# Kernel optimization log

Hardware: AMD Instinct MI355X
Metric: run time of the kernel (lower is better)

Reference implementation:

```python
import jax, jax.numpy as jnp
import numpy as np

N_HEAD = 16
TOPK = 2


def _forward(x, noise, Wk, Wv, Wq, Wo, Wg, Wn):
    B, T, C = x.shape
    E = Wg.shape[1]
    H = N_HEAD
    D = C // H
    x2 = x.reshape(-1, C)  # [N, C], N = B*T
    # noisy gating: logits + randn * softplus(noise_proj)
    gate_logits = x2 @ Wg + noise * jax.nn.softplus(x2 @ Wn)  # [N, E]
    w, sel = jax.lax.top_k(gate_logits, TOPK)                 # [N, K]
    w = jax.nn.softmax(w.astype(jnp.float32), axis=1).astype(x.dtype)
    # shared keys/values across experts
    k = (x @ Wk).reshape(B, T, H, D)
    v = (x @ Wv).reshape(B, T, H, D)
    # per-expert queries for all tokens, gathered per selected expert below
    q_all = jnp.einsum('btc,eco->bteo', x, Wq)  # [B, T, E, C]
    causal = jnp.tril(jnp.ones((T, T), dtype=bool))  # key j visible to query t iff j <= t
    scale = 1.0 / np.sqrt(D).astype(np.float32)
    sel_bt = sel.reshape(B, T, TOPK)
    w_bt = w.reshape(B, T, TOPK)
    out = jnp.zeros_like(x)
    for s in range(TOPK):  # small fixed loop over top-k slots
        e = sel_bt[:, :, s]  # [B, T] expert id per token
        q = jnp.take_along_axis(q_all, e[:, :, None, None], axis=2)[:, :, 0, :]  # [B, T, C]
        qh = q.reshape(B, T, H, D)
        scores = jnp.einsum('bthd,bjhd->bhtj', qh, k) * scale  # [B, H, T, T]
        scores = jnp.where(causal[None, None], scores, -jnp.inf)
        p = jax.nn.softmax(scores, axis=-1)
        attn = jnp.einsum('bhtj,bjhd->bthd', p, v).reshape(B, T, C)
        o_all = jnp.einsum('btc,eco->bteo', attn, Wo)  # [B, T, E, C]
        o = jnp.take_along_axis(o_all, e[:, :, None, None], axis=2)[:, :, 0, :]
        out = out + w_bt[:, :, s:s + 1] * o
    return out


def setup_inputs() -> dict:
    key = jax.random.key(0)
    ks = jax.random.split(key, 8)
    B, T, C, E = 4, 1024, 1024, 8
    s = 0.02
    x = jax.random.normal(ks[0], (B, T, C), jnp.float32)
    noise = jax.random.normal(ks[1], (B * T, E), jnp.float32)
    Wk = jax.random.normal(ks[2], (C, C), jnp.float32) * s
    Wv = jax.random.normal(ks[3], (C, C), jnp.float32) * s
    Wq = jax.random.normal(ks[4], (E, C, C), jnp.float32) * s
    Wo = jax.random.normal(ks[5], (E, C, C), jnp.float32) * s
    Wg = jax.random.normal(ks[6], (C, E), jnp.float32) * s
    Wn = jax.random.normal(ks[7], (C, E), jnp.float32) * s
    return {'x': x, 'noise': noise, 'Wk': Wk, 'Wv': Wv, 'Wq': Wq, 'Wo': Wo, 'Wg': Wg, 'Wn': Wn}


def reference(x, noise, Wk, Wv, Wq, Wo, Wg, Wn):
    return _forward(x, noise, Wk, Wv, Wq, Wo, Wg, Wn)
```

## Files before the change

kernel.cpp:

```cpp
#include <hip/hip_runtime.h>
#include <hip/hip_bf16.h>

#define TSEQ   1024
#define NC     1024
#define MBT    4096
#define NEXP   8
#define NHEAD  16
#define DHEAD  64
#define PERM_CAP 10240
#define MAXTILES 96

typedef __attribute__((ext_vector_type(8))) short bf16x8;
typedef __attribute__((ext_vector_type(4))) float f32x4;

typedef __attribute__((address_space(3))) unsigned char* lds_ptr_t;
typedef const __attribute__((address_space(1))) unsigned char* glb_ptr_t;

static __device__ __forceinline__ void gload16(const void* g, void* l){
    __builtin_amdgcn_global_load_lds((glb_ptr_t)g, (lds_ptr_t)l, 16, 0, 0);
}

static __device__ __forceinline__ unsigned short f2bf(float x){
    unsigned int u = __float_as_uint(x);
    u += 0x7fff + ((u >> 16) & 1);
    return (unsigned short)(u >> 16);
}
static __device__ __forceinline__ unsigned int pk2bf(float a, float b){
    unsigned int ua = __float_as_uint(a), ub = __float_as_uint(b);
    ua += 0x7fff + ((ua >> 16) & 1);
    ub += 0x7fff + ((ub >> 16) & 1);
    return (ua >> 16) | (ub & 0xffff0000u);
}
static __device__ __forceinline__ float bf2f(unsigned short u){
    return __uint_as_float(((unsigned int)u) << 16);
}

__global__ __launch_bounds__(256)
void gate_kernel(const float* __restrict__ x, const float* __restrict__ noise,
                 const float* __restrict__ Wg, const float* __restrict__ Wn,
                 int* __restrict__ epair, float* __restrict__ wpair,
                 unsigned short* __restrict__ xb){
    int t = blockIdx.x*4 + (threadIdx.x >> 6);
    int lane = threadIdx.x & 63;
    float ag[8] = {0,0,0,0,0,0,0,0};
    float an[8] = {0,0,0,0,0,0,0,0};
    const float* xr = x + (size_t)t * NC;
    unsigned short* xbr = xb + (size_t)t * NC;
    for (int c = lane; c < NC; c += 64){
        float xv = xr[c];
        xbr[c] = f2bf(xv);
        #pragma unroll
        for (int j = 0; j < 8; j++){
            ag[j] = fmaf(xv, Wg[c*8 + j], ag[j]);
            an[j] = fmaf(xv, Wn[c*8 + j], an[j]);
        }
    }
    #pragma unroll
    for (int j = 0; j < 8; j++){
        #pragma unroll
        for (int o = 32; o >= 1; o >>= 1){
            ag[j] += __shfl_xor(ag[j], o, 64);
            an[j] += __shfl_xor(an[j], o, 64);
        }
    }
    if (lane == 0){
        float lg[8];
        #pragma unroll
        for (int j = 0; j < 8; j++){
            float z = an[j];
            float sp = (z > 20.f) ? z : log1pf(expf(z));
            lg[j] = ag[j] + noise[(size_t)t*8 + j] * sp;
        }
        int i0 = 0; float v0 = lg[0];
        #pragma unroll
        for (int j = 1; j < 8; j++) if (lg[j] > v0){ v0 = lg[j]; i0 = j; }
        int i1 = -1; float v1 = -3.4e38f;
        #pragma unroll
        for (int j = 0; j < 8; j++) if (j != i0 && lg[j] > v1){ v1 = lg[j]; i1 = j; }
        float e1 = expf(v1 - v0);
        float w0 = 1.f / (1.f + e1);
        epair[2*t]   = i0;
        epair[2*t+1] = i1;
        wpair[2*t]   = w0;
        wpair[2*t+1] = e1 * w0;
    }
}

__global__ void prep_w(const float* __restrict__ Wk, const float* __restrict__ Wv,
                       const float* __restrict__ Wq, const float* __restrict__ Wo,
                       unsigned short* __restrict__ Wkvt, unsigned short* __restrict__ Wqt,
                       unsigned short* __restrict__ Wot){
    __shared__ float t[32][33];
    int z = blockIdx.z;
    const float* src; unsigned short* dst;
    if (z == 0){ src = Wk; dst = Wkvt; }
    else if (z == 1){ src = Wv; dst = Wkvt + (size_t)NC*NC; }
    else if (z < 10){ src = Wq + (size_t)(z-2)*NC*NC; dst = Wqt + (size_t)(z-2)*NC*NC; }
    else { src = Wo + (size_t)(z-10)*NC*NC; dst = Wot + (size_t)(z-10)*NC*NC; }
    int k0 = blockIdx.x * 32, n0 = blockIdx.y * 32;
    int tx = threadIdx.x, ty = threadIdx.y;
    #pragma unroll
    for (int i = 0; i < 4; i++)
        t[ty + i*8][tx] = src[(size_t)(k0 + ty + i*8)*NC + n0 + tx];
    __syncthreads();
    #pragma unroll
    for (int i = 0; i < 4; i++)
        dst[(size_t)(n0 + ty + i*8)*NC + k0 + tx] = f2bf(t[tx][ty + i*8]);
}

__global__ void group_build(const int* __restrict__ epair, int* __restrict__ cursor,
                            int* __restrict__ tile_g, int* __restrict__ tile_pos,
                            int* __restrict__ ntiles, int* __restrict__ perm){
    __shared__ int cnt[16];
    int tid = threadIdx.x;
    if (tid < 16) cnt[tid] = 0;
    __syncthreads();
    for (int p = tid; p < 2*MBT; p += 256){
        int g = ((p & 1) << 3) | epair[p];
        atomicAdd(&cnt[g], 1);
    }
    for (int i = tid; i < PERM_CAP; i += 256) perm[i] = -1;
    __syncthreads();
    if (tid == 0){
        int off = 0, tt = 0;
        for (int g = 0; g < 16; g++){
            int c = cnt[g];
            cursor[g] = off;
            int nt = (c + 127) >> 7;
            for (int i = 0; i < nt; i++){ tile_g[tt] = g; tile_pos[tt] = off + i*128; tt++; }
            off += nt << 7;
        }
        ntiles[0] = tt;
    }
}

__global__ __launch_bounds__(256)
void fill_perm(const int* __restrict__ epair, int* __restrict__ cursor,
               int* __restrict__ perm){
    int p = blockIdx.x * 256 + threadIdx.x;
    int lane = threadIdx.x & 63;
    int g = ((p & 1) << 3) | epair[p];
    unsigned long long ltmask = (lane == 63) ? 0x7fffffffffffffffull
                                             : (((unsigned long long)1 << lane) - 1);
    #pragma unroll 1
    for (int grp = 0; grp < 16; grp++){
        unsigned long long m = __ballot(g == grp);
        if (m == 0ull) continue;
        if (g == grp){
            int leader = __ffsll(m) - 1;
            int base = 0;
            if (lane == leader) base = atomicAdd(&cursor[grp], __popcll(m));
            base = __shfl(base, leader, 64);
            perm[base + __popcll(m & ltmask)] = p;
        }
    }
}

__global__ __launch_bounds__(256)
void gemm_fused(const unsigned short* __restrict__ xb,
                const unsigned short* __restrict__ Wkvt,
                const unsigned short* __restrict__ Wqt,
                unsigned short* __restrict__ kbuf,
                unsigned short* __restrict__ vbT,
                unsigned short* __restrict__ qselb,
                const int* __restrict__ perm,
                const int* __restrict__ tile_g,
                const int* __restrict__ tile_pos,
                const int* __restrict__ ntiles){
    int flat = blockIdx.x;
    bool isQ = (flat >= 512);
    int ntile, slot, tpos = 0;
    const unsigned short* bt;
    if (!isQ){
        ntile = flat & 15; slot = flat >> 4;
        bt = Wkvt;
    } else {
        int f2 = flat - 512;
        ntile = f2 & 7; slot = f2 >> 3;
        if (slot >= ntiles[0]) return;
        int g = tile_g[slot];
        bt = Wqt + (size_t)(g & 7) * NC * NC;
        tpos = tile_pos[slot];
    }

    __shared__ __align__(16) unsigned short smem[16896];
    unsigned short* As = smem;
    unsigned short* Bs = smem + 8192;

    int tid = threadIdx.x;
    int lane = tid & 63, wv = tid >> 6;
    int wr = wv >> 1, wc = wv & 1;
    int quad = lane >> 4, l15 = lane & 15;

    int laneR = lane >> 3;
    int swz = ((lane & 7) ^ (laneR & 7)) * 8;

    const unsigned short* ag[4];
    const unsigned short* bg[4];
    #pragma unroll
    for (int it = 0; it < 4; it++){
        int row = wv*32 + it*8 + laneR;
        if (!isQ){
            ag[it] = xb + (size_t)(slot*128 + row) * NC + swz;
        } else {
            int p = perm[tpos + row];
            if (p < 0) p = 0;
            ag[it] = xb + (size_t)(p >> 1) * NC + swz;
        }
        bg[it] = bt + (size_t)(ntile*128 + row) * NC + swz;
    }

    f32x4 acc[4][4];
    #pragma unroll
    for (int i = 0; i < 4; i++)
        #pragma unroll
        for (int j = 0; j < 4; j++) acc[i][j] = (f32x4){0.f,0.f,0.f,0.f};

    for (int kk = 0; kk < NC; kk += 64){
        #pragma unroll
        for (int it = 0; it < 4; it++){
            gload16(ag[it] + kk, &As[(wv*32 + it*8)*64]);
            gload16(bg[it] + kk, &Bs[(wv*32 + it*8)*64]);
        }
        __syncthreads();
        #pragma unroll
        for (int kh = 0; kh < 2; kh++){
            bf16x8 af[4], bfr[4];
            #pragma unroll
            for (int mi = 0; mi < 4; mi++)
                af[mi]  = *(const bf16x8*)&As[(wr*64 + mi*16 + l15)*64 + (((kh*4 + quad) ^ (l15 & 7))*8)];
            #pragma unroll
            for (int ni = 0; ni < 4; ni++)
                bfr[ni] = *(const bf16x8*)&Bs[(wc*64 + ni*16 + l15)*64 + (((kh*4 + quad) ^ (l15 & 7))*8)];
            #pragma unroll
            for (int mi = 0; mi < 4; mi++)
                #pragma unroll
                for (int ni = 0; ni < 4; ni++)
                    acc[mi][ni] = __builtin_amdgcn_mfma_f32_16x16x32_bf16(af[mi], bfr[ni], acc[mi][ni], 0, 0, 0);
        }
        __syncthreads();
    }

    bool isV = (!isQ) && (ntile >= 8);
    float scale = isQ ? 0.125f : 1.0f;
    if (!isV){
        #pragma unroll
        for (int mi = 0; mi < 4; mi++)
            #pragma unroll
            for (int ni = 0; ni < 4; ni++)
                #pragma unroll
                for (int r = 0; r < 4; r++)
                    smem[(wr*64 + mi*16 + quad*4 + r)*132 + wc*64 + ni*16 + l15] =
                        f2bf(scale * acc[mi][ni][r]);
        __syncthreads();
        #pragma unroll
        for (int cc = 0; cc < 8; cc++){
            int chunk = tid + cc*256;
            int row = chunk >> 4, c8 = (chunk & 15) * 8;
            uint4 v = *(const uint4*)&smem[row*132 + c8];
            if (!isQ){
                *(uint4*)(kbuf + (size_t)(slot*128 + row)*NC + ntile*128 + c8) = v;
            } else {
                int p = perm[tpos + row];
                if (p >= 0)
                    *(uint4*)(qselb + (size_t)p*NC + ntile*128 + c8) = v;
            }
        }
    } else {
        #pragma unroll
        for (int mi = 0; mi < 4; mi++)
            #pragma unroll
            for (int ni = 0; ni < 4; ni++){
                ushort4 pk;
                pk.x = f2bf(acc[mi][ni][0]);
                pk.y = f2bf(acc[mi][ni][1]);
                pk.z = f2bf(acc[mi][ni][2]);
                pk.w = f2bf(acc[mi][ni][3]);
                *(ushort4*)&smem[(wc*64 + ni*16 + l15)*132 + wr*64 + mi*16 + quad*4] = pk;
            }
        __syncthreads();
        int b = slot >> 3, t0 = (slot & 7)*128;
        int cvBase = (ntile - 8)*128;
        #pragma unroll
        for (int cc = 0; cc < 8; cc++){
            int chunk = tid + cc*256;
            int row = chunk >> 4, c8 = (chunk & 15) * 8;
            uint4 v = *(const uint4*)&smem[row*132 + c8];
            *(uint4*)(vbT + ((size_t)(b*NC + cvBase + row))*TSEQ + t0 + c8) = v;
        }
    }
}

__global__ __launch_bounds__(256)
void gemm_o(const unsigned short* __restrict__ A,
            const unsigned short* __restrict__ Bt,
            unsigned short* __restrict__ osb,
            const int* __restrict__ perm,
            const int* __restrict__ tile_g,
            const int* __restrict__ tile_pos,
            const int* __restrict__ ntiles){
    int ntile = blockIdx.x;
    int slot  = blockIdx.y;
    if (slot >= ntiles[0]) return;
    int g = tile_g[slot];
    const unsigned short* bt = Bt + (size_t)(g & 7) * NC * NC;
    int tpos = tile_pos[slot];

    __shared__ __align__(16) unsigned short smem[16896];
    unsigned short* As = smem;
    unsigned short* Bs = smem + 8192;

    int tid = threadIdx.x;
    int lane = tid & 63, wv = tid >> 6;
    int wr = wv >> 1, wc = wv & 1;
    int quad = lane >> 4, l15 = lane & 15;

    int laneR = lane >> 3;
    int swz = ((lane & 7) ^ (laneR & 7)) * 8;

    const unsigned short* ag[4];
    const unsigned short* bg[4];
    #pragma unroll
    for (int it = 0; it < 4; it++){
        int row = wv*32 + it*8 + laneR;
        int p = perm[tpos + row];
        if (p < 0) p = 0;
        ag[it] = A + (size_t)(p & 1) * MBT * NC + (size_t)(p >> 1) * NC + swz;
        bg[it] = bt + (size_t)(ntile*128 + row) * NC + swz;
    }

    f32x4 acc[4][4];
    #pragma unroll
    for (int i = 0; i < 4; i++)
        #pragma unroll
        for (int j = 0; j < 4; j++) acc[i][j] = (f32x4){0.f,0.f,0.f,0.f};

    for (int kk = 0; kk < NC; kk += 64){
        #pragma unroll
        for (int it = 0; it < 4; it++){
            gload16(ag[it] + kk, &As[(wv*32 + it*8)*64]);
            gload16(bg[it] + kk, &Bs[(wv*32 + it*8)*64]);
        }
        __syncthreads();
        #pragma unroll
        for (int kh = 0; kh < 2; kh++){
            bf16x8 af[4], bfr[4];
            #pragma unroll
            for (int mi = 0; mi < 4; mi++)
                af[mi]  = *(const bf16x8*)&As[(wr*64 + mi*16 + l15)*64 + (((kh*4 + quad) ^ (l15 & 7))*8)];
            #pragma unroll
            for (int ni = 0; ni < 4; ni++)
                bfr[ni] = *(const bf16x8*)&Bs[(wc*64 + ni*16 + l15)*64 + (((kh*4 + quad) ^ (l15 & 7))*8)];
            #pragma unroll
            for (int mi = 0; mi < 4; mi++)
                #pragma unroll
                for (int ni = 0; ni < 4; ni++)
                    acc[mi][ni] = __builtin_amdgcn_mfma_f32_16x16x32_bf16(af[mi], bfr[ni], acc[mi][ni], 0, 0, 0);
        }
        __syncthreads();
    }

    #pragma unroll
    for (int mi = 0; mi < 4; mi++)
        #pragma unroll
        for (int ni = 0; ni < 4; ni++)
            #pragma unroll
            for (int r = 0; r < 4; r++)
                smem[(wr*64 + mi*16 + quad*4 + r)*132 + wc*64 + ni*16 + l15] =
                    f2bf(acc[mi][ni][r]);
    __syncthreads();
    #pragma unroll
    for (int cc = 0; cc < 8; cc++){
        int chunk = tid + cc*256;
        int row = chunk >> 4, c8 = (chunk & 15) * 8;
        int p = perm[tpos + row];
        if (p >= 0){
            uint4 v = *(const uint4*)&smem[row*132 + c8];
            *(uint4*)(osb + ((size_t)(p & 1)*MBT + (p >> 1))*NC + ntile*128 + c8) = v;
        }
    }
}

__global__ __launch_bounds__(256)
void combine(const unsigned short* __restrict__ os, const float* __restrict__ wpair,
             float* __restrict__ out){
    size_t flat = ((size_t)blockIdx.x * 256 + threadIdx.x) * 8;
    int t = (int)(flat >> 10);
    float w0 = wpair[2*t], w1 = wpair[2*t+1];
    bf16x8 a = *(const bf16x8*)(os + flat);
    bf16x8 b = *(const bf16x8*)(os + (size_t)MBT*NC + flat);
    float4 r0, r1;
    r0.x = w0*bf2f((unsigned short)a[0]) + w1*bf2f((unsigned short)b[0]);
    r0.y = w0*bf2f((unsigned short)a[1]) + w1*bf2f((unsigned short)b[1]);
    r0.z = w0*bf2f((unsigned short)a[2]) + w1*bf2f((unsigned short)b[2]);
    r0.w = w0*bf2f((unsigned short)a[3]) + w1*bf2f((unsigned short)b[3]);
    r1.x = w0*bf2f((unsigned short)a[4]) + w1*bf2f((unsigned short)b[4]);
    r1.y = w0*bf2f((unsigned short)a[5]) + w1*bf2f((unsigned short)b[5]);
    r1.z = w0*bf2f((unsigned short)a[6]) + w1*bf2f((unsigned short)b[6]);
    r1.w = w0*bf2f((unsigned short)a[7]) + w1*bf2f((unsigned short)b[7]);
    *(float4*)(out + flat)     = r0;
    *(float4*)(out + flat + 4) = r1;
}

__global__ __launch_bounds__(256)
void attn_k(const unsigned short* __restrict__ qsel, const unsigned short* __restrict__ kb,
            const unsigned short* __restrict__ vbT, unsigned short* __restrict__ attnb){
    int b = blockIdx.y >> 4, h = blockIdx.y & 15;
    int s = blockIdx.z;
    int tid = threadIdx.x, lane = tid & 63, wv = tid >> 6;
    int quad = lane >> 4, l15 = lane & 15;
    int laneR = lane >> 3;
    int swz = ((lane & 7) ^ (laneR & 7)) * 8;

    __shared__ __align__(16) unsigned short ksh[64*64];
    __shared__ __align__(16) unsigned short vsh[64*64];
    __shared__ __align__(16) unsigned short pwork[4][32][72];

    #pragma unroll
    for (int half = 0; half < 2; half++){
        int qb = half ? (7 - blockIdx.x) : blockIdx.x;
        int qbase = qb*128 + wv*32;
        int ig[2] = { qbase + l15, qbase + 16 + l15 };

        bf16x8 qf[2][2];
        #pragma unroll
        for (int isub = 0; isub < 2; isub++){
            const unsigned short* qrow = qsel + (((size_t)(b*TSEQ + qbase + isub*16 + l15))*2 + s)*NC + h*DHEAD;
            qf[isub][0] = *(const bf16x8*)(qrow + quad*8);
            qf[isub][1] = *(const bf16x8*)(qrow + 32 + quad*8);
        }

        float lrun[2] = {0.f, 0.f};
        f32x4 oacc[4][2];
        #pragma unroll
        for (int d = 0; d < 4; d++)
            #pragma unroll
            for (int i = 0; i < 2; i++) oacc[d][i] = (f32x4){0.f,0.f,0.f,0.f};

        int njt = qb*2 + 2;
        for (int jt = 0; jt < njt; jt++){
            #pragma unroll
            for (int it = 0; it < 2; it++){
                int r = wv*16 + it*8 + laneR;
                gload16(kb  + ((size_t)(b*TSEQ + jt*64 + r))*NC + h*DHEAD + swz,
                        &ksh[(wv*16 + it*8)*64]);
                gload16(vbT + ((size_t)(b*NC + h*DHEAD + r))*TSEQ + jt*64 + swz,
                        &vsh[(wv*16 + it*8)*64]);
            }
            __syncthreads();

            if (jt*64 <= qbase + 31){
                f32x4 sac[4][2];
                #pragma unroll
                for (int jsub = 0; jsub < 4; jsub++){
                    bf16x8 kf0 = *(const bf16x8*)&ksh[(jsub*16 + l15)*64 + ((quad     ^ (l15 & 7))*8)];
                    bf16x8 kf1 = *(const bf16x8*)&ksh[(jsub*16 + l15)*64 + (((4+quad) ^ (l15 & 7))*8)];
                    #pragma unroll
                    for (int isub = 0; isub < 2; isub++){
                        f32x4 z = (f32x4){0.f,0.f,0.f,0.f};
                        z = __builtin_amdgcn_mfma_f32_16x16x32_bf16(kf0, qf[isub][0], z, 0, 0, 0);
                        z = __builtin_amdgcn_mfma_f32_16x16x32_bf16(kf1, qf[isub][1], z, 0, 0, 0);
                        sac[jsub][isub] = z;
                    }
                }
                if (jt*64 + 63 > qbase){
                    #pragma unroll
                    for (int jsub = 0; jsub < 4; jsub++)
                        #pragma unroll
                        for (int r = 0; r < 4; r++){
                            int j = jt*64 + jsub*16 + quad*4 + r;
                            #pragma unroll
                            for (int isub = 0; isub < 2; isub++)
                                if (j > ig[isub]) sac[jsub][isub][r] = -1e30f;
                        }
                }
                #pragma unroll
                for (int isub = 0; isub < 2; isub++){
                    float rs = 0.f;
                    #pragma unroll
                    for (int jsub = 0; jsub < 4; jsub++){
                        float p0 = __expf(sac[jsub][isub][0]);
                        float p1 = __expf(sac[jsub][isub][1]);
                        float p2 = __expf(sac[jsub][isub][2]);
                        float p3 = __expf(sac[jsub][isub][3]);
                        rs += (p0 + p1) + (p2 + p3);
                        uint2 pk;
                        pk.x = pk2bf(p0, p1);
                        pk.y = pk2bf(p2, p3);
                        *(uint2*)&pwork[wv][isub*16 + l15][jsub*16 + quad*4] = pk;
                    }
                    rs += __shfl_xor(rs, 16, 64);
                    rs += __shfl_xor(rs, 32, 64);
                    lrun[isub] += rs;
                }
                bf16x8 pf[2][2];
                #pragma unroll
                for (int kh = 0; kh < 2; kh++)
                    #pragma unroll
                    for (int isub = 0; isub < 2; isub++)
                        pf[kh][isub] = *(const bf16x8*)&pwork[wv][isub*16 + l15][kh*32 + quad*8];
                #pragma unroll
                for (int dsub = 0; dsub < 4; dsub++){
                    bf16x8 vf0 = *(const bf16x8*)&vsh[(dsub*16 + l15)*64 + ((quad     ^ (l15 & 7))*8)];
                    bf16x8 vf1 = *(const bf16x8*)&vsh[(dsub*16 + l15)*64 + (((4+quad) ^ (l15 & 7))*8)];
                    #pragma unroll
                    for (int isub = 0; isub < 2; isub++){
                        oacc[dsub][isub] = __builtin_amdgcn_mfma_f32_16x16x32_bf16(vf0, pf[0][isub], oacc[dsub][isub], 0, 0, 0);
                        oacc[dsub][isub] = __builtin_amdgcn_mfma_f32_16x16x32_bf16(vf1, pf[1][isub], oacc[dsub][isub], 0, 0, 0);
                    }
                }
            }
            __syncthreads();
        }

        float inv[2] = { 1.f / lrun[0], 1.f / lrun[1] };
        #pragma unroll
        for (int dsub = 0; dsub < 4; dsub++)
            #pragma unroll
            for (int isub = 0; isub < 2; isub++){
                uint2 ov;
                ov.x = pk2bf(oacc[dsub][isub][0] * inv[isub], oacc[dsub][isub][1] * inv[isub]);
                ov.y = pk2bf(oacc[dsub][isub][2] * inv[isub], oacc[dsub][isub][3] * inv[isub]);
                *(uint2*)&pwork[wv][isub*16 + l15][dsub*16 + quad*4] = ov;
            }
        #pragma unroll
        for (int rr = 0; rr < 4; rr++){
            int idx = rr*64 + lane;
            int il = idx >> 3, cc = (idx & 7) * 8;
            int t = qb*128 + wv*32 + il;
            *(uint4*)(attnb + (size_t)s*MBT*NC + ((size_t)(b*TSEQ + t))*NC + h*DHEAD + cc) =
                *(const uint4*)&pwork[wv][il][cc];
        }
    }
}

extern "C" void kernel_launch(void* const* d_in, const int* in_sizes, int n_in,
                              void* d_out, int out_size, void* d_ws, size_t ws_size,
                              hipStream_t stream){
    (void)in_sizes; (void)n_in; (void)out_size; (void)ws_size;
    const float* x     = (const float*)d_in[0];
    const float* noise = (const float*)d_in[1];
    const float* Wk    = (const float*)d_in[2];
    const float* Wv    = (const float*)d_in[3];
    const float* Wq    = (const float*)d_in[4];
    const float* Wo    = (const float*)d_in[5];
    const float* Wg    = (const float*)d_in[6];
    const float* Wn    = (const float*)d_in[7];
    float* out = (float*)d_out;

    char* ws = (char*)d_ws;
    size_t off = 0;
    auto alloc = [&](size_t bytes) -> void* {
        void* p = ws + off;
        off += (bytes + 255) & ~(size_t)255;
        return p;
    };
    unsigned short* xb    = (unsigned short*)alloc((size_t)MBT*NC*2);
    unsigned short* vbufT = (unsigned short*)alloc((size_t)MBT*NC*2);
    unsigned short* kbuf  = (unsigned short*)alloc((size_t)MBT*NC*2);
    unsigned short* qselb = (unsigned short*)alloc((size_t)MBT*2*NC*2);
    unsigned short* attnb = (unsigned short*)alloc((size_t)2*MBT*NC*2);
    unsigned short* Wkvt  = (unsigned short*)alloc((size_t)2*NC*NC*2);
    unsigned short* Wqt   = (unsigned short*)alloc((size_t)NEXP*NC*NC*2);
    unsigned short* Wot   = (unsigned short*)alloc((size_t)NEXP*NC*NC*2);
    int*   epair   = (int*)alloc(2*MBT*4);
    float* wpair   = (float*)alloc(2*MBT*4);
    int*   perm    = (int*)alloc(PERM_CAP*4);
    int*   cursor  = (int*)alloc(16*4);
    int*   tile_g  = (int*)alloc(MAXTILES*4);
    int*   tile_pos= (int*)alloc(MAXTILES*4);
    int*   ntiles  = (int*)alloc(4);

    unsigned short* osb = qselb;

    prep_w<<<dim3(32,32,18), dim3(32,8), 0, stream>>>(Wk, Wv, Wq, Wo, Wkvt, Wqt, Wot);
    gate_kernel<<<1024, 256, 0, stream>>>(x, noise, Wg, Wn, epair, wpair, xb);
    group_build<<<1, 256, 0, stream>>>(epair, cursor, tile_g, tile_pos, ntiles, perm);
    fill_perm<<<32, 256, 0, stream>>>(epair, cursor, perm);

    gemm_fused<<<1280, 256, 0, stream>>>(xb, Wkvt, Wqt, kbuf, vbufT, qselb,
                                         perm, tile_g, tile_pos, ntiles);

    attn_k<<<dim3(4,64,2), 256, 0, stream>>>(qselb, kbuf, vbufT, attnb);

    gemm_o<<<dim3(8,MAXTILES), 256, 0, stream>>>(attnb, Wot, osb, perm, tile_g, tile_pos, ntiles);
    combine<<<2048, 256, 0, stream>>>(osb, wpair, out);
}
```

Before: 347.0 us.

## Double-buffer LDS tiles in GEMM and attention kernels; merge weight prep with gating

```diff
diff --git a/kernel.cpp b/kernel.cpp
--- a/kernel.cpp
+++ b/kernel.cpp
@@ -36,12 +36,37 @@
 }
 
 __global__ __launch_bounds__(256)
-void gate_kernel(const float* __restrict__ x, const float* __restrict__ noise,
-                 const float* __restrict__ Wg, const float* __restrict__ Wn,
-                 int* __restrict__ epair, float* __restrict__ wpair,
-                 unsigned short* __restrict__ xb){
-    int t = blockIdx.x*4 + (threadIdx.x >> 6);
-    int lane = threadIdx.x & 63;
+void prep_gate(const float* __restrict__ Wk, const float* __restrict__ Wv,
+               const float* __restrict__ Wq, const float* __restrict__ Wo,
+               unsigned short* __restrict__ Wkvt, unsigned short* __restrict__ Wqt,
+               unsigned short* __restrict__ Wot,
+               const float* __restrict__ x, const float* __restrict__ noise,
+               const float* __restrict__ Wg, const float* __restrict__ Wn,
+               int* __restrict__ epair, float* __restrict__ wpair,
+               unsigned short* __restrict__ xb){
+    int z = blockIdx.z;
+    int tx = threadIdx.x, ty = threadIdx.y;
+    if (z < 18){
+        __shared__ float t[32][33];
+        const float* src; unsigned short* dst;
+        if (z == 0){ src = Wk; dst = Wkvt; }
+        else if (z == 1){ src = Wv; dst = Wkvt + (size_t)NC*NC; }
+        else if (z < 10){ src = Wq + (size_t)(z-2)*NC*NC; dst = Wqt + (size_t)(z-2)*NC*NC; }
+        else { src = Wo + (size_t)(z-10)*NC*NC; dst = Wot + (size_t)(z-10)*NC*NC; }
+        int k0 = blockIdx.x * 32, n0 = blockIdx.y * 32;
+        #pragma unroll
+        for (int i = 0; i < 4; i++)
+            t[ty + i*8][tx] = src[(size_t)(k0 + ty + i*8)*NC + n0 + tx];
+        __syncthreads();
+        #pragma unroll
+        for (int i = 0; i < 4; i++)
+            dst[(size_t)(n0 + ty + i*8)*NC + k0 + tx] = f2bf(t[tx][ty + i*8]);
+        return;
+    }
+    int flat = ty*32 + tx;
+    int blk = blockIdx.y*32 + blockIdx.x;
+    int t = blk*4 + (flat >> 6);
+    int lane = flat & 63;
     float ag[8] = {0,0,0,0,0,0,0,0};
     float an[8] = {0,0,0,0,0,0,0,0};
     const float* xr = x + (size_t)t * NC;
@@ -67,8 +92,8 @@
         float lg[8];
         #pragma unroll
         for (int j = 0; j < 8; j++){
-            float z = an[j];
-            float sp = (z > 20.f) ? z : log1pf(expf(z));
+            float z2 = an[j];
+            float sp = (z2 > 20.f) ? z2 : log1pf(expf(z2));
             lg[j] = ag[j] + noise[(size_t)t*8 + j] * sp;
         }
         int i0 = 0; float v0 = lg[0];
@@ -84,28 +109,6 @@
         wpair[2*t]   = w0;
         wpair[2*t+1] = e1 * w0;
     }
-}
-
-__global__ void prep_w(const float* __restrict__ Wk, const float* __restrict__ Wv,
-                       const float* __restrict__ Wq, const float* __restrict__ Wo,
-                       unsigned short* __restrict__ Wkvt, unsigned short* __restrict__ Wqt,
-                       unsigned short* __restrict__ Wot){
-    __shared__ float t[32][33];
-    int z = blockIdx.z;
-    const float* src; unsigned short* dst;
-    if (z == 0){ src = Wk; dst = Wkvt; }
-    else if (z == 1){ src = Wv; dst = Wkvt + (size_t)NC*NC; }
-    else if (z < 10){ src = Wq + (size_t)(z-2)*NC*NC; dst = Wqt + (size_t)(z-2)*NC*NC; }
-    else { src = Wo + (size_t)(z-10)*NC*NC; dst = Wot + (size_t)(z-10)*NC*NC; }
-    int k0 = blockIdx.x * 32, n0 = blockIdx.y * 32;
-    int tx = threadIdx.x, ty = threadIdx.y;
-    #pragma unroll
-    for (int i = 0; i < 4; i++)
-        t[ty + i*8][tx] = src[(size_t)(k0 + ty + i*8)*NC + n0 + tx];
-    __syncthreads();
-    #pragma unroll
-    for (int i = 0; i < 4; i++)
-        dst[(size_t)(n0 + ty + i*8)*NC + k0 + tx] = f2bf(t[tx][ty + i*8]);
 }
 
 __global__ void group_build(const int* __restrict__ epair, int* __restrict__ cursor,
@@ -155,6 +158,8 @@
         }
     }
 }
+
+#define AB 8192
 
 __global__ __launch_bounds__(256)
 void gemm_fused(const unsigned short* __restrict__ xb,
@@ -183,10 +188,7 @@
         tpos = tile_pos[slot];
     }
 
-    __shared__ __align__(16) unsigned short smem[16896];
-    unsigned short* As = smem;
-    unsigned short* Bs = smem + 8192;
-
+    __shared__ __align__(16) unsigned short smem[4*AB];
     int tid = threadIdx.x;
     int lane = tid & 63, wv = tid >> 6;
     int wr = wv >> 1, wc = wv & 1;
@@ -216,13 +218,24 @@
         #pragma unroll
         for (int j = 0; j < 4; j++) acc[i][j] = (f32x4){0.f,0.f,0.f,0.f};
 
+    #pragma unroll
+    for (int it = 0; it < 4; it++){
+        gload16(ag[it], &smem[(wv*32 + it*8)*64]);
+        gload16(bg[it], &smem[AB + (wv*32 + it*8)*64]);
+    }
+    int cur = 0;
     for (int kk = 0; kk < NC; kk += 64){
-        #pragma unroll
-        for (int it = 0; it < 4; it++){
-            gload16(ag[it] + kk, &As[(wv*32 + it*8)*64]);
-            gload16(bg[it] + kk, &Bs[(wv*32 + it*8)*64]);
-        }
         __syncthreads();
+        if (kk + 64 < NC){
+            int nb = (cur ^ 1) * 2 * AB;
+            #pragma unroll
+            for (int it = 0; it < 4; it++){
+                gload16(ag[it] + kk + 64, &smem[nb + (wv*32 + it*8)*64]);
+                gload16(bg[it] + kk + 64, &smem[nb + AB + (wv*32 + it*8)*64]);
+            }
+        }
+        const unsigned short* As = &smem[cur*2*AB];
+        const unsigned short* Bs = &smem[cur*2*AB + AB];
         #pragma unroll
         for (int kh = 0; kh < 2; kh++){
             bf16x8 af[4], bfr[4];
@@ -238,8 +251,9 @@
                 for (int ni = 0; ni < 4; ni++)
                     acc[mi][ni] = __builtin_amdgcn_mfma_f32_16x16x32_bf16(af[mi], bfr[ni], acc[mi][ni], 0, 0, 0);
         }
-        __syncthreads();
-    }
+        cur ^= 1;
+    }
+    __syncthreads();
 
     bool isV = (!isQ) && (ntile >= 8);
     float scale = isQ ? 0.125f : 1.0f;
@@ -306,10 +320,7 @@
     const unsigned short* bt = Bt + (size_t)(g & 7) * NC * NC;
     int tpos = tile_pos[slot];
 
-    __shared__ __align__(16) unsigned short smem[16896];
-    unsigned short* As = smem;
-    unsigned short* Bs = smem + 8192;
-
+    __shared__ __align__(16) unsigned short smem[4*AB];
     int tid = threadIdx.x;
     int lane = tid & 63, wv = tid >> 6;
     int wr = wv >> 1, wc = wv & 1;
@@ -335,13 +346,24 @@
         #pragma unroll
         for (int j = 0; j < 4; j++) acc[i][j] = (f32x4){0.f,0.f,0.f,0.f};
 
+    #pragma unroll
+    for (int it = 0; it < 4; it++){
+        gload16(ag[it], &smem[(wv*32 + it*8)*64]);
+        gload16(bg[it], &smem[AB + (wv*32 + it*8)*64]);
+    }
+    int cur = 0;
     for (int kk = 0; kk < NC; kk += 64){
-        #pragma unroll
-        for (int it = 0; it < 4; it++){
-            gload16(ag[it] + kk, &As[(wv*32 + it*8)*64]);
-            gload16(bg[it] + kk, &Bs[(wv*32 + it*8)*64]);
-        }
         __syncthreads();
+        if (kk + 64 < NC){
+            int nb = (cur ^ 1) * 2 * AB;
+            #pragma unroll
+            for (int it = 0; it < 4; it++){
+                gload16(ag[it] + kk + 64, &smem[nb + (wv*32 + it*8)*64]);
+                gload16(bg[it] + kk + 64, &smem[nb + AB + (wv*32 + it*8)*64]);
+            }
+        }
+        const unsigned short* As = &smem[cur*2*AB];
+        const unsigned short* Bs = &smem[cur*2*AB + AB];
         #pragma unroll
         for (int kh = 0; kh < 2; kh++){
             bf16x8 af[4], bfr[4];
@@ -357,8 +379,9 @@
                 for (int ni = 0; ni < 4; ni++)
                     acc[mi][ni] = __builtin_amdgcn_mfma_f32_16x16x32_bf16(af[mi], bfr[ni], acc[mi][ni], 0, 0, 0);
         }
-        __syncthreads();
-    }
+        cur ^= 1;
+    }
+    __syncthreads();
 
     #pragma unroll
     for (int mi = 0; mi < 4; mi++)
@@ -402,6 +425,8 @@
     *(float4*)(out + flat + 4) = r1;
 }
 
+#define KVB 4096
+
 __global__ __launch_bounds__(256)
 void attn_k(const unsigned short* __restrict__ qsel, const unsigned short* __restrict__ kb,
             const unsigned short* __restrict__ vbT, unsigned short* __restrict__ attnb){
@@ -412,8 +437,7 @@
     int laneR = lane >> 3;
     int swz = ((lane & 7) ^ (laneR & 7)) * 8;
 
-    __shared__ __align__(16) unsigned short ksh[64*64];
-    __shared__ __align__(16) unsigned short vsh[64*64];
+    __shared__ __align__(16) unsigned short kv[4*KVB];
     __shared__ __align__(16) unsigned short pwork[4][32][72];
 
     #pragma unroll
@@ -438,79 +462,93 @@
             for (int i = 0; i < 2; i++) oacc[d][i] = (f32x4){0.f,0.f,0.f,0.f};
 
         int njt = qb*2 + 2;
+        __syncthreads();
+        #pragma unroll
+        for (int it = 0; it < 2; it++){
+            int r = wv*16 + it*8 + laneR;
+            gload16(kb  + ((size_t)(b*TSEQ + r))*NC + h*DHEAD + swz,
+                    &kv[(wv*16 + it*8)*64]);
+            gload16(vbT + ((size_t)(b*NC + h*DHEAD + r))*TSEQ + swz,
+                    &kv[2*KVB + (wv*16 + it*8)*64]);
+        }
+        int cur = 0;
         for (int jt = 0; jt < njt; jt++){
-            #pragma unroll
-            for (int it = 0; it < 2; it++){
-                int r = wv*16 + it*8 + laneR;
-                gload16(kb  + ((size_t)(b*TSEQ + jt*64 + r))*NC + h*DHEAD + swz,
-                        &ksh[(wv*16 + it*8)*64]);
-                gload16(vbT + ((size_t)(b*NC + h*DHEAD + r))*TSEQ + jt*64 + swz,
-                        &vsh[(wv*16 + it*8)*64]);
-            }
             __syncthreads();
-
-            if (jt*64 <= qbase + 31){
-                f32x4 sac[4][2];
+            if (jt + 1 < njt){
+                int nb = (cur ^ 1) * KVB;
+                #pragma unroll
+                for (int it = 0; it < 2; it++){
+                    int r = wv*16 + it*8 + laneR;
+                    gload16(kb  + ((size_t)(b*TSEQ + (jt+1)*64 + r))*NC + h*DHEAD + swz,
+                            &kv[nb + (wv*16 + it*8)*64]);
+                    gload16(vbT + ((size_t)(b*NC + h*DHEAD + r))*TSEQ + (jt+1)*64 + swz,
+                            &kv[nb + 2*KVB + (wv*16 + it*8)*64]);
+                }
+            }
+            const unsigned short* ksh = &kv[cur*KVB];
+            const unsigned short* vsh = &kv[cur*KVB + 2*KVB];
+            cur ^= 1;
+
+            if (jt*64 > qbase + 31) continue;
+            f32x4 sac[4][2];
+            #pragma unroll
+            for (int jsub = 0; jsub < 4; jsub++){
+                bf16x8 kf0 = *(const bf16x8*)&ksh[(jsub*16 + l15)*64 + ((quad     ^ (l15 & 7))*8)];
+                bf16x8 kf1 = *(const bf16x8*)&ksh[(jsub*16 + l15)*64 + (((4+quad) ^ (l15 & 7))*8)];
+                #pragma unroll
+                for (int isub = 0; isub < 2; isub++){
+                    f32x4 z = (f32x4){0.f,0.f,0.f,0.f};
+                    z = __builtin_amdgcn_mfma_f32_16x16x32_bf16(kf0, qf[isub][0], z, 0, 0, 0);
+                    z = __builtin_amdgcn_mfma_f32_16x16x32_bf16(kf1, qf[isub][1], z, 0, 0, 0);
+                    sac[jsub][isub] = z;
+                }
+            }
+            if (jt*64 + 63 > qbase){
+                #pragma unroll
+                for (int jsub = 0; jsub < 4; jsub++)
+                    #pragma unroll
+                    for (int r = 0; r < 4; r++){
+                        int j = jt*64 + jsub*16 + quad*4 + r;
+                        #pragma unroll
+                        for (int isub = 0; isub < 2; isub++)
+                            if (j > ig[isub]) sac[jsub][isub][r] = -1e30f;
+                    }
+            }
+            #pragma unroll
+            for (int isub = 0; isub < 2; isub++){
+                float rs = 0.f;
                 #pragma unroll
                 for (int jsub = 0; jsub < 4; jsub++){
-                    bf16x8 kf0 = *(const bf16x8*)&ksh[(jsub*16 + l15)*64 + ((quad     ^ (l15 & 7))*8)];
-                    bf16x8 kf1 = *(const bf16x8*)&ksh[(jsub*16 + l15)*64 + (((4+quad) ^ (l15 & 7))*8)];
-                    #pragma unroll
-                    for (int isub = 0; isub < 2; isub++){
-                        f32x4 z = (f32x4){0.f,0.f,0.f,0.f};
-                        z = __builtin_amdgcn_mfma_f32_16x16x32_bf16(kf0, qf[isub][0], z, 0, 0, 0);
-                        z = __builtin_amdgcn_mfma_f32_16x16x32_bf16(kf1, qf[isub][1], z, 0, 0, 0);
-                        sac[jsub][isub] = z;
-                    }
+                    float p0 = __expf(sac[jsub][isub][0]);
+                    float p1 = __expf(sac[jsub][isub][1]);
+                    float p2 = __expf(sac[jsub][isub][2]);
+                    float p3 = __expf(sac[jsub][isub][3]);
+                    rs += (p0 + p1) + (p2 + p3);
+                    uint2 pk;
+                    pk.x = pk2bf(p0, p1);
+                    pk.y = pk2bf(p2, p3);
+                    *(uint2*)&pwork[wv][isub*16 + l15][jsub*16 + quad*4] = pk;
                 }
-                if (jt*64 + 63 > qbase){
-                    #pragma unroll
-                    for (int jsub = 0; jsub < 4; jsub++)
-                        #pragma unroll
-                        for (int r = 0; r < 4; r++){
-                            int j = jt*64 + jsub*16 + quad*4 + r;
-                            #pragma unroll
-                            for (int isub = 0; isub < 2; isub++)
-                                if (j > ig[isub]) sac[jsub][isub][r] = -1e30f;
-                        }
+                rs += __shfl_xor(rs, 16, 64);
+                rs += __shfl_xor(rs, 32, 64);
+                lrun[isub] += rs;
+            }
+            bf16x8 pf[2][2];
+            #pragma unroll
+            for (int kh = 0; kh < 2; kh++)
+                #pragma unroll
+                for (int isub = 0; isub < 2; isub++)
+                    pf[kh][isub] = *(const bf16x8*)&pwork[wv][isub*16 + l15][kh*32 + quad*8];
+            #pragma unroll
+            for (int dsub = 0; dsub < 4; dsub++){
+                bf16x8 vf0 = *(const bf16x8*)&vsh[(dsub*16 + l15)*64 + ((quad     ^ (l15 & 7))*8)];
+                bf16x8 vf1 = *(const bf16x8*)&vsh[(dsub*16 + l15)*64 + (((4+quad) ^ (l15 & 7))*8)];
+                #pragma unroll
+                for (int isub = 0; isub < 2; isub++){
+                    oacc[dsub][isub] = __builtin_amdgcn_mfma_f32_16x16x32_bf16(vf0, pf[0][isub], oacc[dsub][isub], 0, 0, 0);
+                    oacc[dsub][isub] = __builtin_amdgcn_mfma_f32_16x16x32_bf16(vf1, pf[1][isub], oacc[dsub][isub], 0, 0, 0);
                 }
-                #pragma unroll
-                for (int isub = 0; isub < 2; isub++){
-                    float rs = 0.f;
-                    #pragma unroll
-                    for (int jsub = 0; jsub < 4; jsub++){
-                        float p0 = __expf(sac[jsub][isub][0]);
-                        float p1 = __expf(sac[jsub][isub][1]);
-                        float p2 = __expf(sac[jsub][isub][2]);
-                        float p3 = __expf(sac[jsub][isub][3]);
-                        rs += (p0 + p1) + (p2 + p3);
-                        uint2 pk;
-                        pk.x = pk2bf(p0, p1);
-                        pk.y = pk2bf(p2, p3);
-                        *(uint2*)&pwork[wv][isub*16 + l15][jsub*16 + quad*4] = pk;
-                    }
-                    rs += __shfl_xor(rs, 16, 64);
-                    rs += __shfl_xor(rs, 32, 64);
-                    lrun[isub] += rs;
-                }
-                bf16x8 pf[2][2];
-                #pragma unroll
-                for (int kh = 0; kh < 2; kh++)
-                    #pragma unroll
-                    for (int isub = 0; isub < 2; isub++)
-                        pf[kh][isub] = *(const bf16x8*)&pwork[wv][isub*16 + l15][kh*32 + quad*8];
-                #pragma unroll
-                for (int dsub = 0; dsub < 4; dsub++){
-                    bf16x8 vf0 = *(const bf16x8*)&vsh[(dsub*16 + l15)*64 + ((quad     ^ (l15 & 7))*8)];
-                    bf16x8 vf1 = *(const bf16x8*)&vsh[(dsub*16 + l15)*64 + (((4+quad) ^ (l15 & 7))*8)];
-                    #pragma unroll
-                    for (int isub = 0; isub < 2; isub++){
-                        oacc[dsub][isub] = __builtin_amdgcn_mfma_f32_16x16x32_bf16(vf0, pf[0][isub], oacc[dsub][isub], 0, 0, 0);
-                        oacc[dsub][isub] = __builtin_amdgcn_mfma_f32_16x16x32_bf16(vf1, pf[1][isub], oacc[dsub][isub], 0, 0, 0);
-                    }
-                }
-            }
-            __syncthreads();
+            }
         }
 
         float inv[2] = { 1.f / lrun[0], 1.f / lrun[1] };
@@ -573,8 +611,8 @@
 
     unsigned short* osb = qselb;
 
-    prep_w<<<dim3(32,32,18), dim3(32,8), 0, stream>>>(Wk, Wv, Wq, Wo, Wkvt, Wqt, Wot);
-    gate_kernel<<<1024, 256, 0, stream>>>(x, noise, Wg, Wn, epair, wpair, xb);
+    prep_gate<<<dim3(32,32,19), dim3(32,8), 0, stream>>>(Wk, Wv, Wq, Wo, Wkvt, Wqt, Wot,
+                                                         x, noise, Wg, Wn, epair, wpair, xb);
     group_build<<<1, 256, 0, stream>>>(epair, cursor, tile_g, tile_pos, ntiles, perm);
     fill_perm<<<32, 256, 0, stream>>>(epair, cursor, perm);
 
```

Result: no change. 352.8 us (+1.7%).
